# Kernel tuning notes

Hardware: AMD Instinct MI355X
Metric: run time of the kernel (lower is better)

## Reference

```python
import jax, jax.numpy as jnp
from jax import lax
import numpy as np

# cfg constants (not present in snippet; fixed realistic values)
GAMMA = 5.0            # cfg.RISK_AVERSION
COST_COEFF = 1e-3      # cfg.COST_COEFF
ALPHA = 0.95           # cfg.CVAR_CONFIDENCE
KAPPA = 2.0627128075074256  # norm.pdf(norm.ppf(0.95)) / (1 - 0.95)
PEN_XI = 100.0
N_ITERS = 500
LR = 0.01

B, H, N = 128, 12, 100


def setup_inputs() -> dict:
    key = jax.random.key(0)
    k1, k2, k3, k4 = jax.random.split(key, 4)
    mu = 0.02 * jax.random.normal(k1, (B, H, N), dtype=jnp.float32)
    # factor scale so that sigma_p = ||L^T w|| is O(0.02) for diversified w
    L = 0.02 * jax.random.normal(k2, (B, H, N, N), dtype=jnp.float32)
    w_prev = jax.random.uniform(k3, (B, N), dtype=jnp.float32)
    w_prev = w_prev / jnp.sum(w_prev, axis=-1, keepdims=True)  # on simplex
    cvar_limit = 0.05 + 0.05 * jax.random.uniform(k4, (B,), dtype=jnp.float32)
    return {"mu": mu, "L": L, "w_prev": w_prev, "cvar_limit": cvar_limit}


def _project_simplex(v):
    # Euclidean projection of each last-axis vector onto {w >= 0, sum w = 1}
    n = v.shape[-1]
    u = jnp.sort(v, axis=-1)[..., ::-1]
    cssv = jnp.cumsum(u, axis=-1) - 1.0
    ar = jnp.arange(1, n + 1, dtype=v.dtype)
    rho = jnp.sum(u * ar > cssv, axis=-1)          # >= 1 always
    theta = jnp.take_along_axis(cssv, (rho - 1)[..., None], axis=-1)
    theta = theta / rho[..., None].astype(v.dtype)
    return jnp.maximum(v - theta, 0.0)


def _neg_objective(w, mu, L, w_prev, cvar_limit):
    # w: (B,H,N). Exact-penalty reformulation: optimal xi_t = relu(-mu_p + kappa*sigma_p - limit)
    Lw = jnp.einsum('bhnm,bhn->bhm', L, w)             # L[t].T @ w[t]
    ret_t = jnp.einsum('bhn,bhn->bh', mu, w)           # mu[t] @ w[t]
    risk = jnp.sum(Lw * Lw, axis=(1, 2))               # sum_t ||L_t^T w_t||^2
    w_lag = jnp.concatenate([w_prev[:, None, :], w[:, :-1]], axis=1)
    diff = w - w_lag
    cost = jnp.sum(jnp.sqrt(diff * diff + 1e-10), axis=(1, 2))  # smoothed L1 turnover
    sigma = jnp.sqrt(jnp.sum(Lw * Lw, axis=-1) + 1e-12)          # (B,H)
    viol = jnp.maximum(-ret_t + KAPPA * sigma - cvar_limit[:, None], 0.0)
    obj = jnp.sum(ret_t, 1) - GAMMA * risk - COST_COEFF * cost - PEN_XI * jnp.sum(viol, 1)
    return -jnp.sum(obj)


def _solve(mu, L, w_prev, cvar_limit):
    b, h, n = mu.shape
    w0 = jnp.broadcast_to(w_prev[:, None, :], (b, h, n))
    grad_fn = jax.grad(_neg_objective)

    def step(w, _):
        g = grad_fn(w, mu, L, w_prev, cvar_limit)
        return _project_simplex(w - LR * g), None

    w, _ = lax.scan(jax.checkpoint(step), w0, None, length=N_ITERS)
    return w


def reference(mu, L, w_prev, cvar_limit):
    # Batched projected-gradient solver for the same convex MPO program the
    # original solves with SCS via CvxpyLayer; returns the optimal plan w (B,H,N).
    return _solve(mu, L, w_prev, cvar_limit)
```

## Files before the change

kernel.cpp:

```cpp
#include <hip/hip_runtime.h>
#include <cstdint>
#include <cstddef>

#define NIT    500
#define GAMMA_ 5.0f
#define CC_    1e-3f
#define KAPPA_ 2.0627128075074256f
#define PEN_   100.0f
#define LR_    0.01f

#define PBUF_BYTES (128*2*2*100*4)
#define FLAG_COUNT 256

#define VMFENCE() asm volatile("s_waitcnt vmcnt(0)" ::: "memory")
#define BARRIER() do { asm volatile("s_waitcnt lgkmcnt(0)" ::: "memory"); \
                       __builtin_amdgcn_s_barrier(); } while (0)
__device__ __forceinline__ float sysLoadF(float* p) {
  return __hip_atomic_load(p, __ATOMIC_RELAXED, __HIP_MEMORY_SCOPE_SYSTEM);
}
__device__ __forceinline__ void sysStoreF(float* p, float v) {
  __hip_atomic_store(p, v, __ATOMIC_RELAXED, __HIP_MEMORY_SCOPE_SYSTEM);
}
__device__ __forceinline__ int sysLoadI(int* p) {
  return __hip_atomic_load(p, __ATOMIC_RELAXED, __HIP_MEMORY_SCOPE_SYSTEM);
}
__device__ __forceinline__ void sysStoreI(int* p, int v) {
  __hip_atomic_store(p, v, __ATOMIC_RELAXED, __HIP_MEMORY_SCOPE_SYSTEM);
}
__device__ __forceinline__ int flagRead(int* p, int lane) {
  int f = 0;
  if (lane == 0) f = sysLoadI(p);
  return __builtin_amdgcn_readfirstlane(f);
}
__device__ __forceinline__ int ldsLoadAcq(int* p) {
  return __hip_atomic_load(p, __ATOMIC_ACQUIRE, __HIP_MEMORY_SCOPE_WORKGROUP);
}
__device__ __forceinline__ void ldsStoreRel(int* p, int v) {
  __hip_atomic_store(p, v, __ATOMIC_RELEASE, __HIP_MEMORY_SCOPE_WORKGROUP);
}

__device__ __forceinline__ float rdlane(float v, int lane) {
  return __int_as_float(__builtin_amdgcn_readlane(__float_as_int(v), lane));
}

__device__ __forceinline__ float wred64(float x) {
  int t;
  t = __builtin_amdgcn_update_dpp(0, __float_as_int(x), 0x111, 0xf, 0xf, true); x += __int_as_float(t);
  t = __builtin_amdgcn_update_dpp(0, __float_as_int(x), 0x112, 0xf, 0xf, true); x += __int_as_float(t);
  t = __builtin_amdgcn_update_dpp(0, __float_as_int(x), 0x114, 0xf, 0xf, true); x += __int_as_float(t);
  t = __builtin_amdgcn_update_dpp(0, __float_as_int(x), 0x118, 0xf, 0xf, true); x += __int_as_float(t);
  t = __builtin_amdgcn_update_dpp(0, __float_as_int(x), 0x142, 0xa, 0xf, true); x += __int_as_float(t);
  t = __builtin_amdgcn_update_dpp(0, __float_as_int(x), 0x143, 0xc, 0xf, true); x += __int_as_float(t);
  return rdlane(x, 63);
}

__global__ __launch_bounds__(768, 1) void mpo_solver(
    const float* __restrict__ mu, const float* __restrict__ L,
    const float* __restrict__ wprev, const float* __restrict__ climit,
    float* __restrict__ out, float* __restrict__ pbuf, int* __restrict__ flags)
{
  const int tid  = threadIdx.x;
  const int lane = tid & 63;
  const int wave = __builtin_amdgcn_readfirstlane(tid >> 6);
  const int j    = wave >> 1;
  const int sec  = wave & 1;
  const int bid  = blockIdx.x;
  const int b    = bid & 127;
  const int half = bid >> 7;
  const int h    = half * 6 + j;
  const int bh   = b * 12 + h;

  __shared__ float wbuf[2][6][100];
  __shared__ float ybuf[6][100];
  __shared__ float nbuf[100];
  __shared__ int   nflag;

  const float* Lb = L + (size_t)bh * 10000;

  float S[100];
#pragma unroll
  for (int c = 0; c < 100; ++c) S[c] = 0.f;
  const int r = sec * 50 + lane;
  if (lane < 50) {
#pragma unroll 1
    for (int mc = 0; mc < 25; ++mc) {
      float4 lr = *(const float4*)(Lb + r * 100 + mc * 4);
#pragma unroll
      for (int c = 0; c < 100; ++c) {
        const float* Lc = Lb + c * 100 + mc * 4;
        S[c] = fmaf(lr.x, Lc[0], fmaf(lr.y, Lc[1], fmaf(lr.z, Lc[2], fmaf(lr.w, Lc[3], S[c]))));
      }
    }
  }

  const bool val1 = (lane < 36);
  float mu0 = mu[(size_t)bh * 100 + lane];
  float mu1 = val1 ? mu[(size_t)bh * 100 + 64 + lane] : 0.f;
  float wp0 = wprev[b * 100 + lane];
  float wp1 = val1 ? wprev[b * 100 + 64 + lane] : 0.f;
  float lim = climit[b];

  float w0 = wp0, w1 = wp1;

  if (sec == 0) {
    wbuf[0][j][lane] = wp0;
    if (val1) wbuf[0][j][64 + lane] = wp1;
  }
  if (tid == 0) nflag = 0;
  __syncthreads();

  const bool hasNext = (h < 11);
  const bool isPubL  = (half == 0) && (j == 5);
  const bool isPubH  = (half == 1) && (j == 0);
  const bool isBnd   = isPubL || isPubH;
  const int  flagPub = isPubL ? (b * 2 + 0) : (b * 2 + 1);
  const int  flagCon = isPubL ? (b * 2 + 1) : (b * 2 + 0);
  bool dead = false;
  float thp = -3.0e38f;

  for (int k = 0; k < NIT; ++k) {
    const int p = k & 1;

    if (sec == 0 && isBnd && k > 0) {
      VMFENCE();
      if (lane == 0) sysStoreI(&flags[flagPub], k);
    }

    float ret = 0.f;
    if (sec == 0) ret = wred64(fmaf(mu0, w0, mu1 * w1));

    float yloc;
    {
      float a0 = 0.f, a1 = 0.f, a2 = 0.f, a3 = 0.f;
      const float* wrow = wbuf[p][j];
#pragma unroll
      for (int q = 0; q < 25; ++q) {
        float4 wq = *(const float4*)(wrow + q * 4);
        a0 = fmaf(wq.x, S[q * 4 + 0], a0);
        a1 = fmaf(wq.y, S[q * 4 + 1], a1);
        a2 = fmaf(wq.z, S[q * 4 + 2], a2);
        a3 = fmaf(wq.w, S[q * 4 + 3], a3);
      }
      yloc = (a0 + a2) + (a1 + a3);
      if (sec == 1 && lane < 50) ybuf[j][50 + lane] = yloc;
    }
    BARRIER();

    if (sec == 1) {
      if (isBnd && k > 0) {
        if (!dead) {
          long guard = 0;
          while (flagRead(&flags[flagCon], lane) < k) {
            __builtin_amdgcn_s_sleep(1);
            if (++guard > (1L << 18)) { dead = true; break; }
          }
        }
        float* src = pbuf + ((size_t)flagCon * 2 + (k & 1)) * 100;
        nbuf[lane] = sysLoadF(&src[lane]);
        if (val1) nbuf[64 + lane] = sysLoadF(&src[64 + lane]);
        ldsStoreRel(&nflag, k);
      }
    } else {
      float y0 = (lane < 50) ? yloc : ybuf[j][lane];
      float y1 = val1 ? ybuf[j][64 + lane] : 0.f;

      float s2  = wred64(fmaf(y0, w0, y1 * w1));
      float sigma = sqrtf(s2 + 1e-12f);
      float z     = KAPPA_ * sigma - ret - lim;
      float act   = (z > 0.f) ? 1.f : 0.f;
      float cY    = 2.f * GAMMA_ + act * (PEN_ * KAPPA_ / sigma);
      float cM    = -(1.f + act * PEN_);

      float wl0, wl1, wn0 = 0.f, wn1 = 0.f;
      if (j == 0) {
        if (half == 0 || k == 0) { wl0 = wp0; wl1 = wp1; }
        else {
          if (!dead) {
            long guard = 0;
            while (ldsLoadAcq(&nflag) < k) {
              __builtin_amdgcn_s_sleep(1);
              if (++guard > (1L << 18)) { dead = true; break; }
            }
          }
          wl0 = nbuf[lane];
          wl1 = val1 ? nbuf[64 + lane] : 0.f;
        }
      } else { wl0 = wbuf[p][j - 1][lane]; wl1 = val1 ? wbuf[p][j - 1][64 + lane] : 0.f; }
      if (hasNext) {
        if (j == 5) {
          if (k == 0) { wn0 = wp0; wn1 = wp1; }
          else {
            if (!dead) {
              long guard = 0;
              while (ldsLoadAcq(&nflag) < k) {
                __builtin_amdgcn_s_sleep(1);
                if (++guard > (1L << 18)) { dead = true; break; }
              }
            }
            wn0 = nbuf[lane];
            wn1 = val1 ? nbuf[64 + lane] : 0.f;
          }
        } else { wn0 = wbuf[p][j + 1][lane]; wn1 = val1 ? wbuf[p][j + 1][64 + lane] : 0.f; }
      }

      float dw0 = w0 - wl0;
      float g0  = fmaf(cM, mu0, cY * y0) + CC_ * (dw0 * rsqrtf(fmaf(dw0, dw0, 1e-10f)));
      if (hasNext) { float dn0 = wn0 - w0; g0 -= CC_ * (dn0 * rsqrtf(fmaf(dn0, dn0, 1e-10f))); }
      float v0 = fmaf(-LR_, g0, w0);
      float v1 = 0.f;
      if (val1) {
        float dw1 = w1 - wl1;
        float g1  = fmaf(cM, mu1, cY * y1) + CC_ * (dw1 * rsqrtf(fmaf(dw1, dw1, 1e-10f)));
        if (hasNext) { float dn1 = wn1 - w1; g1 -= CC_ * (dn1 * rsqrtf(fmaf(dn1, dn1, 1e-10f))); }
        v1 = fmaf(-LR_, g1, w1);
      }

      float a1m = val1 ? 1.f : 0.f;
      {
        bool c0 = (v0 > thp);
        bool c1 = (val1 && (v1 > thp));
        float Ssum = wred64((c0 ? v0 : 0.f) + (c1 ? v1 : 0.f));
        float Cnt  = (float)(__popcll(__ballot(c0)) + __popcll(__ballot(c1)));
        if (Cnt < 0.5f) { Ssum = wred64(v0 + a1m * v1); Cnt = 100.f; }
        float theta = (Ssum - 1.f) / Cnt;
        for (int it = 0; it < 112; ++it) {
          bool b0 = (v0 > theta);
          bool b1 = (val1 && (v1 > theta));
          float ns = wred64((b0 ? v0 : 0.f) + (b1 ? v1 : 0.f));
          float nc = (float)(__popcll(__ballot(b0)) + __popcll(__ballot(b1)));
          if (nc == Cnt && ns == Ssum) break;
          if (it == 7) {
            ns = wred64(v0 + a1m * v1);
            nc = 100.f;
          }
          Ssum = ns; Cnt = nc;
          theta = (Ssum - 1.f) / Cnt;
        }
        thp = theta;
        w0 = fmaxf(v0 - theta, 0.f);
        w1 = val1 ? fmaxf(v1 - theta, 0.f) : 0.f;
      }

      wbuf[1 - p][j][lane] = w0;
      if (val1) wbuf[1 - p][j][64 + lane] = w1;

      if (isBnd) {
        float* dst = pbuf + ((size_t)flagPub * 2 + ((k + 1) & 1)) * 100;
        sysStoreF(&dst[lane], w0);
        if (val1) sysStoreF(&dst[64 + lane], w1);
      }
    }
    BARRIER();
  }

  if (sec == 0) {
    float* o = out + (size_t)bh * 100;
    o[lane] = w0;
    if (val1) o[64 + lane] = w1;
  }
}

extern "C" void kernel_launch(void* const* d_in, const int* in_sizes, int n_in,
                              void* d_out, int out_size, void* d_ws, size_t ws_size,
                              hipStream_t stream) {
  const float* mu = (const float*)d_in[0];
  const float* L  = (const float*)d_in[1];
  const float* wp = (const float*)d_in[2];
  const float* cl = (const float*)d_in[3];
  float* pbuf  = (float*)d_ws;
  int*   flags = (int*)((char*)d_ws + PBUF_BYTES);
  hipMemsetAsync(flags, 0, FLAG_COUNT * sizeof(int), stream);
  hipLaunchKernelGGL(mpo_solver, dim3(256), dim3(768), 0, stream,
                     mu, L, wp, cl, (float*)d_out, pbuf, flags);
}
```

Baseline: 1.663 ms.

## Move cross-block halo wait before matvec and publish flag right after store

The boundary wave now polls the neighbour block's flag and loads its halo weights at the start of each iteration, before the local matvec. The data reaches LDS through the existing barrier, so the LDS nflag acquire/release spin is removed. The publishing wave now sets its global flag right after storing the new weights, instead of at the start of the next iteration. This cuts the latency on the inter-block dependency chain, but the matvec of the polling wave may now wait behind the spin.

```diff
diff --git a/kernel.cpp b/kernel.cpp
--- a/kernel.cpp
+++ b/kernel.cpp
@@ -31,12 +31,6 @@
   int f = 0;
   if (lane == 0) f = sysLoadI(p);
   return __builtin_amdgcn_readfirstlane(f);
-}
-__device__ __forceinline__ int ldsLoadAcq(int* p) {
-  return __hip_atomic_load(p, __ATOMIC_ACQUIRE, __HIP_MEMORY_SCOPE_WORKGROUP);
-}
-__device__ __forceinline__ void ldsStoreRel(int* p, int v) {
-  __hip_atomic_store(p, v, __ATOMIC_RELEASE, __HIP_MEMORY_SCOPE_WORKGROUP);
 }
 
 __device__ __forceinline__ float rdlane(float v, int lane) {
@@ -73,7 +67,6 @@
   __shared__ float wbuf[2][6][100];
   __shared__ float ybuf[6][100];
   __shared__ float nbuf[100];
-  __shared__ int   nflag;
 
   const float* Lb = L + (size_t)bh * 10000;
 
@@ -106,7 +99,6 @@
     wbuf[0][j][lane] = wp0;
     if (val1) wbuf[0][j][64 + lane] = wp1;
   }
-  if (tid == 0) nflag = 0;
   __syncthreads();
 
   const bool hasNext = (h < 11);
@@ -121,9 +113,18 @@
   for (int k = 0; k < NIT; ++k) {
     const int p = k & 1;
 
-    if (sec == 0 && isBnd && k > 0) {
-      VMFENCE();
-      if (lane == 0) sysStoreI(&flags[flagPub], k);
+    float x0 = 0.f, x1 = 0.f;
+    if (sec == 1 && isBnd && k > 0) {
+      if (!dead) {
+        long guard = 0;
+        while (flagRead(&flags[flagCon], lane) < k) {
+          __builtin_amdgcn_s_sleep(1);
+          if (++guard > (1L << 18)) { dead = true; break; }
+        }
+      }
+      float* src = pbuf + ((size_t)flagCon * 2 + (k & 1)) * 100;
+      x0 = sysLoadF(&src[lane]);
+      if (val1) x1 = sysLoadF(&src[64 + lane]);
     }
 
     float ret = 0.f;
@@ -142,25 +143,17 @@
         a3 = fmaf(wq.w, S[q * 4 + 3], a3);
       }
       yloc = (a0 + a2) + (a1 + a3);
-      if (sec == 1 && lane < 50) ybuf[j][50 + lane] = yloc;
+    }
+    if (sec == 1) {
+      if (lane < 50) ybuf[j][50 + lane] = yloc;
+      if (isBnd && k > 0) {
+        nbuf[lane] = x0;
+        if (val1) nbuf[64 + lane] = x1;
+      }
     }
     BARRIER();
 
-    if (sec == 1) {
-      if (isBnd && k > 0) {
-        if (!dead) {
-          long guard = 0;
-          while (flagRead(&flags[flagCon], lane) < k) {
-            __builtin_amdgcn_s_sleep(1);
-            if (++guard > (1L << 18)) { dead = true; break; }
-          }
-        }
-        float* src = pbuf + ((size_t)flagCon * 2 + (k & 1)) * 100;
-        nbuf[lane] = sysLoadF(&src[lane]);
-        if (val1) nbuf[64 + lane] = sysLoadF(&src[64 + lane]);
-        ldsStoreRel(&nflag, k);
-      }
-    } else {
+    if (sec == 0) {
       float y0 = (lane < 50) ? yloc : ybuf[j][lane];
       float y1 = val1 ? ybuf[j][64 + lane] : 0.f;
 
@@ -175,13 +168,6 @@
       if (j == 0) {
         if (half == 0 || k == 0) { wl0 = wp0; wl1 = wp1; }
         else {
-          if (!dead) {
-            long guard = 0;
-            while (ldsLoadAcq(&nflag) < k) {
-              __builtin_amdgcn_s_sleep(1);
-              if (++guard > (1L << 18)) { dead = true; break; }
-            }
-          }
           wl0 = nbuf[lane];
           wl1 = val1 ? nbuf[64 + lane] : 0.f;
         }
@@ -190,13 +176,6 @@
         if (j == 5) {
           if (k == 0) { wn0 = wp0; wn1 = wp1; }
           else {
-            if (!dead) {
-              long guard = 0;
-              while (ldsLoadAcq(&nflag) < k) {
-                __builtin_amdgcn_s_sleep(1);
-                if (++guard > (1L << 18)) { dead = true; break; }
-              }
-            }
             wn0 = nbuf[lane];
             wn1 = val1 ? nbuf[64 + lane] : 0.f;
           }
@@ -248,6 +227,8 @@
         float* dst = pbuf + ((size_t)flagPub * 2 + ((k + 1) & 1)) * 100;
         sysStoreF(&dst[lane], w0);
         if (val1) sysStoreF(&dst[64 + lane], w1);
+        VMFENCE();
+        if (lane == 0) sysStoreI(&flags[flagPub], k + 1);
       }
     }
     BARRIER();
```

New measurement: 1.789 ms. 1.08x slower.
